# Kernel optimization log

Hardware: AMD Instinct MI355X
Metric: run time of the kernel (lower is better)

## Reference

```python
import jax, jax.numpy as jnp
import numpy as np

B, T, E, H = 64, 577, 768, 64
GRID_H, GRID_W = 24, 24
NUM_PREFIX = 1
N = GRID_H * GRID_W  # 576 patches
EPS = 1e-5


def setup_inputs() -> dict:
    key = jax.random.key(0)
    ks = jax.random.split(key, 12)
    s = lambda k, shape, fan: jax.random.normal(k, shape, jnp.float32) / np.sqrt(fan)
    return {
        "x": jax.random.normal(ks[0], (B, T, E), jnp.float32),
        "w_q": s(ks[1], (E, H), E),
        "w_k": s(ks[2], (E, H), E),
        "w_v": s(ks[3], (E, H), E),
        "q_gamma": jnp.ones((H,), jnp.float32),
        "q_beta": jnp.zeros((H,), jnp.float32),
        "k_gamma": jnp.ones((H,), jnp.float32),
        "k_beta": jnp.zeros((H,), jnp.float32),
        "w_sigma": s(ks[4], (H, 2), H),
        "b_sigma": jnp.zeros((2,), jnp.float32),
        "w_alpha": s(ks[5], (H, 1), H),
        "b_alpha": jnp.zeros((1,), jnp.float32),
    }


def _layernorm(x, gamma, beta):
    mu = jnp.mean(x, axis=-1, keepdims=True)
    var = jnp.mean(jnp.square(x - mu), axis=-1, keepdims=True)
    return (x - mu) * jax.lax.rsqrt(var + EPS) * gamma + beta


def _grid_sq_dists():
    # coords[i] = (row, col) of patch i; squared coordinate differences [N, N]
    coords = jnp.stack(
        jnp.meshgrid(jnp.arange(GRID_H), jnp.arange(GRID_W), indexing="ij"), axis=-1
    ).reshape(N, 2).astype(jnp.float32)
    diff = coords[:, None, :] - coords[None, :, :]  # [N, N, 2]
    dy2 = jnp.square(diff[..., 0])  # row diff squared
    dx2 = jnp.square(diff[..., 1])  # col diff squared
    return dx2, dy2


def reference(x, w_q, w_k, w_v, q_gamma, q_beta, k_gamma, k_beta,
              w_sigma, b_sigma, w_alpha, b_alpha):
    q = _layernorm(x @ w_q, q_gamma, q_beta)  # [B, T, H]
    k = _layernorm(x @ w_k, k_gamma, k_beta)  # [B, T, H]
    v = x @ w_v                               # [B, T, H]

    sim = jnp.einsum("bqh,bkh->bqk", q, k)    # [B, T, T]

    q_nc = q[:, NUM_PREFIX:, :]               # [B, N, H]
    alpha = jax.nn.softplus(q_nc @ w_alpha + b_alpha)[..., 0]  # [B, N]
    sigma = jax.nn.sigmoid(q_nc @ w_sigma + b_sigma)           # [B, N, 2]
    sx = sigma[..., 0]  # [B, N]
    sy = sigma[..., 1]

    dx2, dy2 = _grid_sq_dists()  # [N, N] each
    # Gaussian decay bias: query-patch p controls sigma; [B, N, N]
    G = jnp.exp(
        -dx2[None] / (2.0 * jnp.square(sx)[:, :, None])
        - dy2[None] / (2.0 * jnp.square(sy)[:, :, None])
    )
    S = alpha[:, :, None] * G

    sim = sim.at[:, NUM_PREFIX:, NUM_PREFIX:].add(S)

    scale = jnp.sqrt(jnp.float32(H))
    attn = jax.nn.softmax(sim / scale, axis=-1)
    return attn @ v  # [B, T, H]
```

## Files before the change

### kernel.cpp

```cpp
#include <hip/hip_runtime.h>
#include <math.h>

#define B_ 64
#define T_ 577
#define E_ 768
#define H_ 64
#define N_ 576
#define GW_ 24

typedef float f32x4 __attribute__((ext_vector_type(4)));
typedef __bf16 bf16x8 __attribute__((ext_vector_type(8)));
typedef __bf16 bf16x4 __attribute__((ext_vector_type(4)));

__device__ inline void split_bf16(float f, __bf16& h, __bf16& l) {
  h = (__bf16)f;
  l = (__bf16)(f - (float)h);
}

__device__ inline float bperm_f(int byte_addr, float x) {
  return __int_as_float(__builtin_amdgcn_ds_bpermute(byte_addr, __float_as_int(x)));
}

__global__ __launch_bounds__(256) void prep_w_kernel(
    const float* __restrict__ wq, const float* __restrict__ wk, const float* __restrict__ wv,
    __bf16* __restrict__ wsw_hi, __bf16* __restrict__ wsw_lo)
{
  int t = blockIdx.x * 256 + threadIdx.x;
  if (t >= 24*192) return;
  int kc = t / 192, n = t - (t/192)*192;
  const float* src = (n < 64) ? wq : ((n < 128) ? wk : wv);
  int nn = n & 63;
  __bf16 hbuf[32], lbuf[32];
  #pragma unroll
  for (int kk = 0; kk < 32; ++kk) {
    float f = src[(size_t)(kc*32 + kk)*64 + nn];
    split_bf16(f, hbuf[kk], lbuf[kk]);
  }
  size_t base = (size_t)t * 32;
  #pragma unroll
  for (int i = 0; i < 4; ++i) {
    *(bf16x8*)(wsw_hi + base + i*8) = *(bf16x8*)&hbuf[i*8];
    *(bf16x8*)(wsw_lo + base + i*8) = *(bf16x8*)&lbuf[i*8];
  }
}

__global__ __launch_bounds__(256) void qkv_ln_kernel(
    const float* __restrict__ x,
    const __bf16* __restrict__ wsw_hi, const __bf16* __restrict__ wsw_lo,
    const float* __restrict__ qg, const float* __restrict__ qb,
    const float* __restrict__ kg, const float* __restrict__ kb,
    const float* __restrict__ wsig, const float* __restrict__ bsig,
    const float* __restrict__ walp, const float* __restrict__ balp,
    float* __restrict__ qo, float* __restrict__ ko, float* __restrict__ vo,
    float* __restrict__ alo, float* __restrict__ sxo, float* __restrict__ syo)
{
  __shared__ __align__(16) float smem[64*193 + 256];
  __bf16* A_hi = (__bf16*)smem;
  __bf16* A_lo = A_hi + 64*40;
  __bf16* B_hi = A_lo + 64*40;
  __bf16* B_lo = B_hi + 192*40;
  float (*Cs)[193] = (float (*)[193])smem;
  float* mu_q = smem + 64*193;
  float* rs_q = mu_q + 64;
  float* mu_k = rs_q + 64;
  float* rs_k = mu_k + 64;

  const int tid  = threadIdx.x;
  const int lane = tid & 63;
  const int w    = tid >> 6;
  const int rowbase = blockIdx.x << 6;

  f32x4 acc[4][3];
  #pragma unroll
  for (int mt = 0; mt < 4; ++mt)
    #pragma unroll
    for (int nt = 0; nt < 3; ++nt)
      acc[mt][nt] = (f32x4){0.f, 0.f, 0.f, 0.f};

  const int m     = lane & 15;
  const int kfrag = (lane >> 4) * 8;

  float4 xr0, xr1;
  bf16x8 whr[3], wlr[3];
  const int s0 = tid, s1 = tid + 256;
  const int arow0 = s0 >> 3, ak0 = (s0 & 7) * 4;
  const int arow1 = s1 >> 3, ak1 = (s1 & 7) * 4;

  auto load_chunk = [&](int kc) {
    xr0 = *(const float4*)(x + (size_t)(rowbase + arow0)*E_ + kc*32 + ak0);
    xr1 = *(const float4*)(x + (size_t)(rowbase + arow1)*E_ + kc*32 + ak1);
    #pragma unroll
    for (int i = 0; i < 3; ++i) {
      int e = tid + 256*i;
      whr[i] = *(const bf16x8*)(wsw_hi + (size_t)kc*6144 + e*8);
      wlr[i] = *(const bf16x8*)(wsw_lo + (size_t)kc*6144 + e*8);
    }
  };
  auto store_chunk = [&]() {
    __bf16 h0,l0,h1,l1,h2,l2,h3,l3;
    split_bf16(xr0.x,h0,l0); split_bf16(xr0.y,h1,l1);
    split_bf16(xr0.z,h2,l2); split_bf16(xr0.w,h3,l3);
    *(bf16x4*)&A_hi[arow0*40 + ak0] = (bf16x4){h0,h1,h2,h3};
    *(bf16x4*)&A_lo[arow0*40 + ak0] = (bf16x4){l0,l1,l2,l3};
    split_bf16(xr1.x,h0,l0); split_bf16(xr1.y,h1,l1);
    split_bf16(xr1.z,h2,l2); split_bf16(xr1.w,h3,l3);
    *(bf16x4*)&A_hi[arow1*40 + ak1] = (bf16x4){h0,h1,h2,h3};
    *(bf16x4*)&A_lo[arow1*40 + ak1] = (bf16x4){l0,l1,l2,l3};
    #pragma unroll
    for (int i = 0; i < 3; ++i) {
      int e = tid + 256*i;
      int n = e >> 2, g = e & 3;
      *(bf16x8*)&B_hi[n*40 + g*8] = whr[i];
      *(bf16x8*)&B_lo[n*40 + g*8] = wlr[i];
    }
  };

  load_chunk(0);
  #pragma unroll 1
  for (int kc = 0; kc < 24; ++kc) {
    __syncthreads();
    store_chunk();
    __syncthreads();
    if (kc < 23) load_chunk(kc + 1);

    bf16x8 bh[3], bl[3];
    #pragma unroll
    for (int nt = 0; nt < 3; ++nt) {
      int n = w*48 + nt*16 + m;
      bh[nt] = *(const bf16x8*)&B_hi[n*40 + kfrag];
      bl[nt] = *(const bf16x8*)&B_lo[n*40 + kfrag];
    }
    #pragma unroll
    for (int mt = 0; mt < 4; ++mt) {
      bf16x8 ah = *(const bf16x8*)&A_hi[(mt*16 + m)*40 + kfrag];
      bf16x8 al = *(const bf16x8*)&A_lo[(mt*16 + m)*40 + kfrag];
      #pragma unroll
      for (int nt = 0; nt < 3; ++nt) {
        acc[mt][nt] = __builtin_amdgcn_mfma_f32_16x16x32_bf16(ah, bh[nt], acc[mt][nt], 0, 0, 0);
        acc[mt][nt] = __builtin_amdgcn_mfma_f32_16x16x32_bf16(al, bh[nt], acc[mt][nt], 0, 0, 0);
        acc[mt][nt] = __builtin_amdgcn_mfma_f32_16x16x32_bf16(ah, bl[nt], acc[mt][nt], 0, 0, 0);
      }
    }
  }
  __syncthreads();

  #pragma unroll
  for (int mt = 0; mt < 4; ++mt)
    #pragma unroll
    for (int nt = 0; nt < 3; ++nt) {
      int row = mt*16 + (lane >> 4)*4;
      int col = w*48 + nt*16 + (lane & 15);
      Cs[row + 0][col] = acc[mt][nt].x;
      Cs[row + 1][col] = acc[mt][nt].y;
      Cs[row + 2][col] = acc[mt][nt].z;
      Cs[row + 3][col] = acc[mt][nt].w;
    }
  __syncthreads();

  if (tid < 64) {
    float s = 0.f;
    for (int h = 0; h < 64; ++h) s += Cs[tid][h];
    float mu = s * (1.f/64.f);
    float vs = 0.f;
    for (int h = 0; h < 64; ++h) { float d = Cs[tid][h] - mu; vs += d*d; }
    mu_q[tid] = mu;
    rs_q[tid] = rsqrtf(vs*(1.f/64.f) + 1e-5f);
  } else if (tid < 128) {
    int r = tid - 64;
    float s = 0.f;
    for (int h = 0; h < 64; ++h) s += Cs[r][64+h];
    float mu = s * (1.f/64.f);
    float vs = 0.f;
    for (int h = 0; h < 64; ++h) { float d = Cs[r][64+h] - mu; vs += d*d; }
    mu_k[r] = mu;
    rs_k[r] = rsqrtf(vs*(1.f/64.f) + 1e-5f);
  }
  __syncthreads();

  if (tid >= 192) {
    int r = tid - 192;
    int mrow = rowbase + r;
    int tindex = mrow % T_;
    if (tindex >= 1) {
      int bb = mrow / T_;
      int g = tindex - 1;
      float mu = mu_q[r], rs = rs_q[r];
      float za = 0.f, z0 = 0.f, z1 = 0.f;
      for (int h = 0; h < 64; ++h) {
        float qv = (Cs[r][h] - mu) * rs * qg[h] + qb[h];
        za += qv * walp[h];
        z0 += qv * wsig[2*h];
        z1 += qv * wsig[2*h+1];
      }
      za += balp[0]; z0 += bsig[0]; z1 += bsig[1];
      float al = fmaxf(za, 0.f) + log1pf(__expf(-fabsf(za)));
      float sx = 1.f/(1.f + __expf(-z0));
      float sy = 1.f/(1.f + __expf(-z1));
      alo[bb*N_ + g] = al;
      sxo[bb*N_ + g] = 0.5f/(sx*sx);
      syo[bb*N_ + g] = 0.5f/(sy*sy);
    }
  }
  for (int idx = tid; idx < 64*48; idx += 256) {
    int r = idx / 48, c4 = (idx - (idx/48)*48) * 4;
    size_t row = (size_t)rowbase + r;
    float4 val = make_float4(Cs[r][c4], Cs[r][c4+1], Cs[r][c4+2], Cs[r][c4+3]);
    if (c4 < 64) {
      float mu = mu_q[r], rs = rs_q[r];
      float4 o;
      o.x = (val.x - mu)*rs*qg[c4+0] + qb[c4+0];
      o.y = (val.y - mu)*rs*qg[c4+1] + qb[c4+1];
      o.z = (val.z - mu)*rs*qg[c4+2] + qb[c4+2];
      o.w = (val.w - mu)*rs*qg[c4+3] + qb[c4+3];
      *(float4*)(qo + row*64 + c4) = o;
    } else if (c4 < 128) {
      int h = c4 - 64;
      float mu = mu_k[r], rs = rs_k[r];
      float4 o;
      o.x = (val.x - mu)*rs*kg[h+0] + kb[h+0];
      o.y = (val.y - mu)*rs*kg[h+1] + kb[h+1];
      o.z = (val.z - mu)*rs*kg[h+2] + kb[h+2];
      o.w = (val.w - mu)*rs*kg[h+3] + kb[h+3];
      *(float4*)(ko + row*64 + h) = o;
    } else {
      *(float4*)(vo + row*64 + (c4-128)) = val;
    }
  }
}

__global__ __launch_bounds__(256, 4) void attn_kernel(
    const float* __restrict__ q, const float* __restrict__ k, const float* __restrict__ v,
    const float* __restrict__ ala, const float* __restrict__ sxa, const float* __restrict__ sya,
    float* __restrict__ out)
{
  __shared__ __align__(16) __bf16 sm[4*4608];
  __bf16* KH = sm;            __bf16* KL = sm + 4608;
  __bf16* VH = sm + 2*4608;   __bf16* VL = sm + 3*4608;

  const int tid  = threadIdx.x;
  const int lane = tid & 63;
  const int w    = tid >> 6;
  const int quad = lane >> 4;
  const int m    = lane & 15;
  const int b    = blockIdx.y;
  const int qt   = blockIdx.x;

  const float* qbase = q + (size_t)b * T_ * H_;
  const float* kbase = k + (size_t)b * T_ * H_;
  const float* vbase = v + (size_t)b * T_ * H_;

  const int  row    = qt*64 + w*16 + m;
  const int  rowc   = row < T_ ? row : T_ - 1;
  const bool qvalid = row < T_;
  const bool qhas   = (row >= 1) && qvalid;
  float al = 0.f, isx = 0.f, isy = 0.f, qr = 0.f, qc = 0.f;
  {
    int g = qhas ? row - 1 : 0;
    if (qhas) {
      al  = ala[b*N_ + g] * 0.125f;
      isx = sxa[b*N_ + g];
      isy = sya[b*N_ + g];
      int gr = g / GW_;
      qr = (float)gr;
      qc = (float)(g - gr*GW_);
    }
  }

  bf16x8 qh[2], ql[2];
  #pragma unroll
  for (int ks = 0; ks < 2; ++ks) {
    float4 f0 = *(const float4*)(qbase + (size_t)rowc*H_ + ks*32 + quad*8);
    float4 f1 = *(const float4*)(qbase + (size_t)rowc*H_ + ks*32 + quad*8 + 4);
    float fv[8] = {f0.x, f0.y, f0.z, f0.w, f1.x, f1.y, f1.z, f1.w};
    #pragma unroll
    for (int j = 0; j < 8; ++j) {
      float s = fv[j] * 0.125f;
      __bf16 h, l;
      split_bf16(s, h, l);
      qh[ks][j] = h;
      ql[ks][j] = l;
    }
  }

  float mo = -INFINITY, lsum = 0.f;
  f32x4 acc[4];
  #pragma unroll
  for (int nt = 0; nt < 4; ++nt) acc[nt] = (f32x4){0.f, 0.f, 0.f, 0.f};

  const int  addrA = ((2*(quad & 1))*16 + m) * 4;
  const int  addrB = addrA + 64;
  const bool hiNT  = quad >= 2;

  float4 kreg[4];
  float  vreg[16];
  const int d0 = tid & 15, k0 = (tid >> 4) * 4;

  auto load_kv = [&](int kt) {
    #pragma unroll
    for (int i = 0; i < 4; ++i) {
      int s = tid + 256*i;
      int key = s >> 4, c4 = (s & 15)*4;
      int kgl = kt*64 + key;
      int kcl = kgl < T_ ? kgl : T_ - 1;
      kreg[i] = *(const float4*)(kbase + (size_t)kcl*H_ + c4);
    }
    #pragma unroll
    for (int di = 0; di < 4; ++di)
      #pragma unroll
      for (int ki = 0; ki < 4; ++ki) {
        int kgl = kt*64 + k0 + ki;
        int kcl = kgl < T_ ? kgl : T_ - 1;
        vreg[di*4+ki] = vbase[(size_t)kcl*H_ + d0 + 16*di];
      }
  };
  auto store_kv = [&]() {
    #pragma unroll
    for (int i = 0; i < 4; ++i) {
      int s = tid + 256*i;
      int key = s >> 4, c4 = (s & 15)*4;
      __bf16 h0,l0,h1,l1,h2,l2,h3,l3;
      split_bf16(kreg[i].x,h0,l0); split_bf16(kreg[i].y,h1,l1);
      split_bf16(kreg[i].z,h2,l2); split_bf16(kreg[i].w,h3,l3);
      *(bf16x4*)&KH[key*72 + c4] = (bf16x4){h0,h1,h2,h3};
      *(bf16x4*)&KL[key*72 + c4] = (bf16x4){l0,l1,l2,l3};
    }
    #pragma unroll
    for (int di = 0; di < 4; ++di) {
      int dim = d0 + 16*di;
      __bf16 h0,l0,h1,l1,h2,l2,h3,l3;
      split_bf16(vreg[di*4+0],h0,l0); split_bf16(vreg[di*4+1],h1,l1);
      split_bf16(vreg[di*4+2],h2,l2); split_bf16(vreg[di*4+3],h3,l3);
      *(bf16x4*)&VH[dim*72 + k0] = (bf16x4){h0,h1,h2,h3};
      *(bf16x4*)&VL[dim*72 + k0] = (bf16x4){l0,l1,l2,l3};
    }
  };

  load_kv(0);
  #pragma unroll 1
  for (int kt = 0; kt < 10; ++kt) {
    __syncthreads();
    store_kv();
    __syncthreads();
    if (kt < 9) load_kv(kt + 1);

    float s_[4][4];
    #pragma unroll
    for (int nt = 0; nt < 4; ++nt) {
      f32x4 sac = (f32x4){0.f, 0.f, 0.f, 0.f};
      #pragma unroll
      for (int ks = 0; ks < 2; ++ks) {
        const int ko_ = ks*32 + quad*8;
        bf16x8 kh = *(const bf16x8*)&KH[(nt*16 + m)*72 + ko_];
        bf16x8 kl = *(const bf16x8*)&KL[(nt*16 + m)*72 + ko_];
        sac = __builtin_amdgcn_mfma_f32_16x16x32_bf16(kh, qh[ks], sac, 0, 0, 0);
        sac = __builtin_amdgcn_mfma_f32_16x16x32_bf16(kl, qh[ks], sac, 0, 0, 0);
        sac = __builtin_amdgcn_mfma_f32_16x16x32_bf16(kh, ql[ks], sac, 0, 0, 0);
      }
      s_[nt][0] = sac.x; s_[nt][1] = sac.y; s_[nt][2] = sac.z; s_[nt][3] = sac.w;
    }

    #pragma unroll
    for (int nt = 0; nt < 4; ++nt) {
      #pragma unroll
      for (int reg = 0; reg < 4; ++reg) {
        int key = kt*64 + nt*16 + quad*4 + reg;
        float sval = s_[nt][reg];
        float kgf = (float)(key - 1);
        float krf = floorf(kgf * (1.0f/24.0f));
        float kcf = kgf - 24.f*krf;
        float dx = qc - kcf, dy = qr - krf;
        float bias = al * __expf(-(dx*dx*isx + dy*dy*isy));
        bool khas = (key >= 1) && (key < T_);
        sval += (khas && qhas) ? bias : 0.f;
        s_[nt][reg] = (key < T_) ? sval : -1e30f;
      }
    }

    float mx = s_[0][0];
    #pragma unroll
    for (int nt = 0; nt < 4; ++nt)
      #pragma unroll
      for (int reg = 0; reg < 4; ++reg)
        mx = fmaxf(mx, s_[nt][reg]);
    mx = fmaxf(mx, __shfl_xor(mx, 16, 64));
    mx = fmaxf(mx, __shfl_xor(mx, 32, 64));
    float mn = fmaxf(mo, mx);
    float sc = __expf(mo - mn);
    float lt = 0.f;
    #pragma unroll
    for (int nt = 0; nt < 4; ++nt)
      #pragma unroll
      for (int reg = 0; reg < 4; ++reg) {
        float p = __expf(s_[nt][reg] - mn);
        s_[nt][reg] = p;
        lt += p;
      }
    lt += __shfl_xor(lt, 16, 64);
    lt += __shfl_xor(lt, 32, 64);
    lsum = lsum*sc + lt;
    mo = mn;
    #pragma unroll
    for (int nt = 0; nt < 4; ++nt) {
      acc[nt].x *= sc; acc[nt].y *= sc; acc[nt].z *= sc; acc[nt].w *= sc;
    }

    bf16x8 fh[2], fl[2];
    #pragma unroll
    for (int ks = 0; ks < 2; ++ks) {
      #pragma unroll
      for (int reg = 0; reg < 4; ++reg) {
        float xa0 = bperm_f(addrA, s_[2*ks+0][reg]);
        float xa1 = bperm_f(addrA, s_[2*ks+1][reg]);
        float xb0 = bperm_f(addrB, s_[2*ks+0][reg]);
        float xb1 = bperm_f(addrB, s_[2*ks+1][reg]);
        float va = hiNT ? xa1 : xa0;
        float vb = hiNT ? xb1 : xb0;
        __bf16 h, l;
        split_bf16(va, h, l); fh[ks][reg]   = h; fl[ks][reg]   = l;
        split_bf16(vb, h, l); fh[ks][4+reg] = h; fl[ks][4+reg] = l;
      }
    }

    #pragma unroll
    for (int nt = 0; nt < 4; ++nt) {
      f32x4 c = acc[nt];
      #pragma unroll
      for (int ks = 0; ks < 2; ++ks) {
        const int ko_ = ks*32 + quad*8;
        bf16x8 vh = *(const bf16x8*)&VH[(nt*16 + m)*72 + ko_];
        bf16x8 vl = *(const bf16x8*)&VL[(nt*16 + m)*72 + ko_];
        c = __builtin_amdgcn_mfma_f32_16x16x32_bf16(vh, fh[ks], c, 0, 0, 0);
        c = __builtin_amdgcn_mfma_f32_16x16x32_bf16(vl, fh[ks], c, 0, 0, 0);
        c = __builtin_amdgcn_mfma_f32_16x16x32_bf16(vh, fl[ks], c, 0, 0, 0);
      }
      acc[nt] = c;
    }
  }

  if (qvalid) {
    float inv = 1.f / lsum;
    #pragma unroll
    for (int nt = 0; nt < 4; ++nt) {
      float4 o;
      o.x = acc[nt].x * inv;
      o.y = acc[nt].y * inv;
      o.z = acc[nt].z * inv;
      o.w = acc[nt].w * inv;
      *(float4*)(out + ((size_t)b*T_ + row)*H_ + nt*16 + quad*4) = o;
    }
  }
}

extern "C" void kernel_launch(void* const* d_in, const int* in_sizes, int n_in,
                              void* d_out, int out_size, void* d_ws, size_t ws_size,
                              hipStream_t stream) {
  const float* x      = (const float*)d_in[0];
  const float* wq     = (const float*)d_in[1];
  const float* wk     = (const float*)d_in[2];
  const float* wv     = (const float*)d_in[3];
  const float* qg     = (const float*)d_in[4];
  const float* qb     = (const float*)d_in[5];
  const float* kg     = (const float*)d_in[6];
  const float* kb     = (const float*)d_in[7];
  const float* wsig   = (const float*)d_in[8];
  const float* bsig   = (const float*)d_in[9];
  const float* walp   = (const float*)d_in[10];
  const float* balp   = (const float*)d_in[11];
  float* out = (float*)d_out;

  float* ws  = (float*)d_ws;
  const size_t nrow = (size_t)B_ * T_;
  float* qo  = ws;
  float* ko  = qo + nrow*H_;
  float* vo  = ko + nrow*H_;
  float* alo = vo + nrow*H_;
  float* sxo = alo + (size_t)B_*N_;
  float* syo = sxo + (size_t)B_*N_;
  __bf16* wsw_hi = (__bf16*)(syo + (size_t)B_*N_);
  __bf16* wsw_lo = wsw_hi + 24*192*32;

  hipLaunchKernelGGL(prep_w_kernel, dim3(18), dim3(256), 0, stream,
                     wq, wk, wv, wsw_hi, wsw_lo);
  hipLaunchKernelGGL(qkv_ln_kernel, dim3(577), dim3(256), 0, stream,
                     x, wsw_hi, wsw_lo, qg, qb, kg, kb, wsig, bsig, walp, balp,
                     qo, ko, vo, alo, sxo, syo);
  hipLaunchKernelGGL(attn_kernel, dim3(10, B_), dim3(256), 0, stream,
                     qo, ko, vo, alo, sxo, syo, out);
}
```

Baseline: 292.5 us.

## Load MFMA fragments directly from global memory and swizzle attention block order

```diff
diff --git a/kernel.cpp b/kernel.cpp
--- a/kernel.cpp
+++ b/kernel.cpp
@@ -26,25 +26,28 @@
     __bf16* __restrict__ wsw_hi, __bf16* __restrict__ wsw_lo)
 {
   int t = blockIdx.x * 256 + threadIdx.x;
-  if (t >= 24*192) return;
-  int kc = t / 192, n = t - (t/192)*192;
-  const float* src = (n < 64) ? wq : ((n < 128) ? wk : wv);
-  int nn = n & 63;
-  __bf16 hbuf[32], lbuf[32];
+  if (t >= 24*4*3*64) return;
+  int lane  = t & 63;
+  int rest  = t >> 6;
+  int nt    = rest % 3;
+  int rest2 = rest / 3;
+  int w     = rest2 & 3;
+  int ksl   = rest2 >> 2;
+  int col = w*48 + nt*16 + (lane & 15);
+  int k0  = ksl*32 + (lane >> 4)*8;
+  const float* src = (col < 64) ? wq : ((col < 128) ? wk : wv);
+  int cc = col & 63;
+  __bf16 hb[8], lb[8];
   #pragma unroll
-  for (int kk = 0; kk < 32; ++kk) {
-    float f = src[(size_t)(kc*32 + kk)*64 + nn];
-    split_bf16(f, hbuf[kk], lbuf[kk]);
-  }
-  size_t base = (size_t)t * 32;
-  #pragma unroll
-  for (int i = 0; i < 4; ++i) {
-    *(bf16x8*)(wsw_hi + base + i*8) = *(bf16x8*)&hbuf[i*8];
-    *(bf16x8*)(wsw_lo + base + i*8) = *(bf16x8*)&lbuf[i*8];
-  }
-}
-
-__global__ __launch_bounds__(256) void qkv_ln_kernel(
+  for (int j = 0; j < 8; ++j) {
+    float f = src[(size_t)(k0 + j)*64 + cc];
+    split_bf16(f, hb[j], lb[j]);
+  }
+  *(bf16x8*)(wsw_hi + (size_t)t*8) = *(bf16x8*)hb;
+  *(bf16x8*)(wsw_lo + (size_t)t*8) = *(bf16x8*)lb;
+}
+
+__global__ __launch_bounds__(256, 3) void qkv_ln_kernel(
     const float* __restrict__ x,
     const __bf16* __restrict__ wsw_hi, const __bf16* __restrict__ wsw_lo,
     const float* __restrict__ qg, const float* __restrict__ qb,
@@ -55,10 +58,6 @@
     float* __restrict__ alo, float* __restrict__ sxo, float* __restrict__ syo)
 {
   __shared__ __align__(16) float smem[64*193 + 256];
-  __bf16* A_hi = (__bf16*)smem;
-  __bf16* A_lo = A_hi + 64*40;
-  __bf16* B_hi = A_lo + 64*40;
-  __bf16* B_lo = B_hi + 192*40;
   float (*Cs)[193] = (float (*)[193])smem;
   float* mu_q = smem + 64*193;
   float* rs_q = mu_q + 64;
@@ -68,6 +67,8 @@
   const int tid  = threadIdx.x;
   const int lane = tid & 63;
   const int w    = tid >> 6;
+  const int quad = lane >> 4;
+  const int m    = lane & 15;
   const int rowbase = blockIdx.x << 6;
 
   f32x4 acc[4][3];
@@ -77,63 +78,33 @@
     for (int nt = 0; nt < 3; ++nt)
       acc[mt][nt] = (f32x4){0.f, 0.f, 0.f, 0.f};
 
-  const int m     = lane & 15;
-  const int kfrag = (lane >> 4) * 8;
-
-  float4 xr0, xr1;
-  bf16x8 whr[3], wlr[3];
-  const int s0 = tid, s1 = tid + 256;
-  const int arow0 = s0 >> 3, ak0 = (s0 & 7) * 4;
-  const int arow1 = s1 >> 3, ak1 = (s1 & 7) * 4;
-
-  auto load_chunk = [&](int kc) {
-    xr0 = *(const float4*)(x + (size_t)(rowbase + arow0)*E_ + kc*32 + ak0);
-    xr1 = *(const float4*)(x + (size_t)(rowbase + arow1)*E_ + kc*32 + ak1);
-    #pragma unroll
-    for (int i = 0; i < 3; ++i) {
-      int e = tid + 256*i;
-      whr[i] = *(const bf16x8*)(wsw_hi + (size_t)kc*6144 + e*8);
-      wlr[i] = *(const bf16x8*)(wsw_lo + (size_t)kc*6144 + e*8);
-    }
-  };
-  auto store_chunk = [&]() {
-    __bf16 h0,l0,h1,l1,h2,l2,h3,l3;
-    split_bf16(xr0.x,h0,l0); split_bf16(xr0.y,h1,l1);
-    split_bf16(xr0.z,h2,l2); split_bf16(xr0.w,h3,l3);
-    *(bf16x4*)&A_hi[arow0*40 + ak0] = (bf16x4){h0,h1,h2,h3};
-    *(bf16x4*)&A_lo[arow0*40 + ak0] = (bf16x4){l0,l1,l2,l3};
-    split_bf16(xr1.x,h0,l0); split_bf16(xr1.y,h1,l1);
-    split_bf16(xr1.z,h2,l2); split_bf16(xr1.w,h3,l3);
-    *(bf16x4*)&A_hi[arow1*40 + ak1] = (bf16x4){h0,h1,h2,h3};
-    *(bf16x4*)&A_lo[arow1*40 + ak1] = (bf16x4){l0,l1,l2,l3};
-    #pragma unroll
-    for (int i = 0; i < 3; ++i) {
-      int e = tid + 256*i;
-      int n = e >> 2, g = e & 3;
-      *(bf16x8*)&B_hi[n*40 + g*8] = whr[i];
-      *(bf16x8*)&B_lo[n*40 + g*8] = wlr[i];
-    }
-  };
-
-  load_chunk(0);
-  #pragma unroll 1
-  for (int kc = 0; kc < 24; ++kc) {
-    __syncthreads();
-    store_chunk();
-    __syncthreads();
-    if (kc < 23) load_chunk(kc + 1);
-
+  const __bf16* bbase_h = wsw_hi + ((size_t)w*3*64 + lane)*8;
+  const __bf16* bbase_l = wsw_lo + ((size_t)w*3*64 + lane)*8;
+  const float*  abase   = x + (size_t)(rowbase + m)*E_ + quad*8;
+
+  #pragma unroll 2
+  for (int ks = 0; ks < 24; ++ks) {
     bf16x8 bh[3], bl[3];
     #pragma unroll
     for (int nt = 0; nt < 3; ++nt) {
-      int n = w*48 + nt*16 + m;
-      bh[nt] = *(const bf16x8*)&B_hi[n*40 + kfrag];
-      bl[nt] = *(const bf16x8*)&B_lo[n*40 + kfrag];
+      size_t off = ((size_t)ks*12 + nt)*64*8;
+      bh[nt] = *(const bf16x8*)(bbase_h + off);
+      bl[nt] = *(const bf16x8*)(bbase_l + off);
     }
     #pragma unroll
     for (int mt = 0; mt < 4; ++mt) {
-      bf16x8 ah = *(const bf16x8*)&A_hi[(mt*16 + m)*40 + kfrag];
-      bf16x8 al = *(const bf16x8*)&A_lo[(mt*16 + m)*40 + kfrag];
+      const float* xp = abase + (size_t)mt*16*E_ + ks*32;
+      float4 f0 = *(const float4*)xp;
+      float4 f1 = *(const float4*)(xp + 4);
+      float fv[8] = {f0.x, f0.y, f0.z, f0.w, f1.x, f1.y, f1.z, f1.w};
+      bf16x8 ah, al;
+      #pragma unroll
+      for (int j = 0; j < 8; ++j) {
+        __bf16 h, l;
+        split_bf16(fv[j], h, l);
+        ah[j] = h;
+        al[j] = l;
+      }
       #pragma unroll
       for (int nt = 0; nt < 3; ++nt) {
         acc[mt][nt] = __builtin_amdgcn_mfma_f32_16x16x32_bf16(ah, bh[nt], acc[mt][nt], 0, 0, 0);
@@ -142,14 +113,13 @@
       }
     }
   }
-  __syncthreads();
 
   #pragma unroll
   for (int mt = 0; mt < 4; ++mt)
     #pragma unroll
     for (int nt = 0; nt < 3; ++nt) {
-      int row = mt*16 + (lane >> 4)*4;
-      int col = w*48 + nt*16 + (lane & 15);
+      int row = mt*16 + quad*4;
+      int col = w*48 + nt*16 + m;
       Cs[row + 0][col] = acc[mt][nt].x;
       Cs[row + 1][col] = acc[mt][nt].y;
       Cs[row + 2][col] = acc[mt][nt].z;
@@ -242,8 +212,11 @@
   const int w    = tid >> 6;
   const int quad = lane >> 4;
   const int m    = lane & 15;
-  const int b    = blockIdx.y;
-  const int qt   = blockIdx.x;
+
+  const int f       = blockIdx.y * 10 + blockIdx.x;
+  const int logical = (f & 7) * 80 + (f >> 3);
+  const int b       = logical / 10;
+  const int qt      = logical - b * 10;
 
   const float* qbase = q + (size_t)b * T_ * H_;
   const float* kbase = k + (size_t)b * T_ * H_;
@@ -479,7 +452,7 @@
   __bf16* wsw_hi = (__bf16*)(syo + (size_t)B_*N_);
   __bf16* wsw_lo = wsw_hi + 24*192*32;
 
-  hipLaunchKernelGGL(prep_w_kernel, dim3(18), dim3(256), 0, stream,
+  hipLaunchKernelGGL(prep_w_kernel, dim3(72), dim3(256), 0, stream,
                      wq, wk, wv, wsw_hi, wsw_lo);
   hipLaunchKernelGGL(qkv_ln_kernel, dim3(577), dim3(256), 0, stream,
                      x, wsw_hi, wsw_lo, qg, qb, kg, kb, wsig, bsig, walp, balp,
```

After: 317.1 us. +8.4%, slower.

## Double-buffer QKV GEMM prefetch, parallelize LayerNorm stats, remap attention blocks across XCDs

Applied to the files above, without the earlier changes.

```diff
diff --git a/kernel.cpp b/kernel.cpp
--- a/kernel.cpp
+++ b/kernel.cpp
@@ -20,6 +20,12 @@
 __device__ inline float bperm_f(int byte_addr, float x) {
   return __int_as_float(__builtin_amdgcn_ds_bpermute(byte_addr, __float_as_int(x)));
 }
+
+#define BAR_LGKM() do {                                      \
+    asm volatile("s_waitcnt lgkmcnt(0)" ::: "memory");       \
+    __builtin_amdgcn_s_barrier();                            \
+    asm volatile("" ::: "memory");                           \
+  } while (0)
 
 __global__ __launch_bounds__(256) void prep_w_kernel(
     const float* __restrict__ wq, const float* __restrict__ wk, const float* __restrict__ wv,
@@ -54,13 +60,13 @@
     float* __restrict__ qo, float* __restrict__ ko, float* __restrict__ vo,
     float* __restrict__ alo, float* __restrict__ sxo, float* __restrict__ syo)
 {
-  __shared__ __align__(16) float smem[64*193 + 256];
+  __shared__ __align__(16) float smem[10240];
   __bf16* A_hi = (__bf16*)smem;
   __bf16* A_lo = A_hi + 64*40;
   __bf16* B_hi = A_lo + 64*40;
   __bf16* B_lo = B_hi + 192*40;
-  float (*Cs)[193] = (float (*)[193])smem;
-  float* mu_q = smem + 64*193;
+  float (*Cs)[132] = (float (*)[132])smem;
+  float* mu_q = smem + 64*132;
   float* rs_q = mu_q + 64;
   float* mu_k = rs_q + 64;
   float* rs_k = mu_k + 64;
@@ -68,6 +74,8 @@
   const int tid  = threadIdx.x;
   const int lane = tid & 63;
   const int w    = tid >> 6;
+  const int quad = lane >> 4;
+  const int m    = lane & 15;
   const int rowbase = blockIdx.x << 6;
 
   f32x4 acc[4][3];
@@ -77,51 +85,55 @@
     for (int nt = 0; nt < 3; ++nt)
       acc[mt][nt] = (f32x4){0.f, 0.f, 0.f, 0.f};
 
-  const int m     = lane & 15;
-  const int kfrag = (lane >> 4) * 8;
-
-  float4 xr0, xr1;
-  bf16x8 whr[3], wlr[3];
-  const int s0 = tid, s1 = tid + 256;
-  const int arow0 = s0 >> 3, ak0 = (s0 & 7) * 4;
-  const int arow1 = s1 >> 3, ak1 = (s1 & 7) * 4;
-
-  auto load_chunk = [&](int kc) {
-    xr0 = *(const float4*)(x + (size_t)(rowbase + arow0)*E_ + kc*32 + ak0);
-    xr1 = *(const float4*)(x + (size_t)(rowbase + arow1)*E_ + kc*32 + ak1);
+  const int kfrag = quad * 8;
+
+  float4 xrA0, xrA1, xrB0, xrB1;
+  bf16x8 whA[3], wlA[3], whB[3], wlB[3];
+  const int arow0 = tid >> 3, ak0 = (tid & 7) * 4;
+  const int arow1 = (tid + 256) >> 3, ak1 = (tid & 7) * 4;
+
+  auto load_set = [&](int kc, float4& x0, float4& x1, bf16x8* wh, bf16x8* wl) {
+    x0 = *(const float4*)(x + (size_t)(rowbase + arow0)*E_ + kc*32 + ak0);
+    x1 = *(const float4*)(x + (size_t)(rowbase + arow1)*E_ + kc*32 + ak1);
     #pragma unroll
     for (int i = 0; i < 3; ++i) {
       int e = tid + 256*i;
-      whr[i] = *(const bf16x8*)(wsw_hi + (size_t)kc*6144 + e*8);
-      wlr[i] = *(const bf16x8*)(wsw_lo + (size_t)kc*6144 + e*8);
+      wh[i] = *(const bf16x8*)(wsw_hi + (size_t)kc*6144 + e*8);
+      wl[i] = *(const bf16x8*)(wsw_lo + (size_t)kc*6144 + e*8);
     }
   };
-  auto store_chunk = [&]() {
+  auto store_set = [&](float4& x0, float4& x1, bf16x8* wh, bf16x8* wl) {
     __bf16 h0,l0,h1,l1,h2,l2,h3,l3;
-    split_bf16(xr0.x,h0,l0); split_bf16(xr0.y,h1,l1);
-    split_bf16(xr0.z,h2,l2); split_bf16(xr0.w,h3,l3);
+    split_bf16(x0.x,h0,l0); split_bf16(x0.y,h1,l1);
+    split_bf16(x0.z,h2,l2); split_bf16(x0.w,h3,l3);
     *(bf16x4*)&A_hi[arow0*40 + ak0] = (bf16x4){h0,h1,h2,h3};
     *(bf16x4*)&A_lo[arow0*40 + ak0] = (bf16x4){l0,l1,l2,l3};
-    split_bf16(xr1.x,h0,l0); split_bf16(xr1.y,h1,l1);
-    split_bf16(xr1.z,h2,l2); split_bf16(xr1.w,h3,l3);
+    split_bf16(x1.x,h0,l0); split_bf16(x1.y,h1,l1);
+    split_bf16(x1.z,h2,l2); split_bf16(x1.w,h3,l3);
     *(bf16x4*)&A_hi[arow1*40 + ak1] = (bf16x4){h0,h1,h2,h3};
     *(bf16x4*)&A_lo[arow1*40 + ak1] = (bf16x4){l0,l1,l2,l3};
     #pragma unroll
     for (int i = 0; i < 3; ++i) {
       int e = tid + 256*i;
       int n = e >> 2, g = e & 3;
-      *(bf16x8*)&B_hi[n*40 + g*8] = whr[i];
-      *(bf16x8*)&B_lo[n*40 + g*8] = wlr[i];
+      *(bf16x8*)&B_hi[n*40 + g*8] = wh[i];
+      *(bf16x8*)&B_lo[n*40 + g*8] = wl[i];
     }
   };
 
-  load_chunk(0);
+  load_set(0, xrA0, xrA1, whA, wlA);
+  load_set(1, xrB0, xrB1, whB, wlB);
+
   #pragma unroll 1
   for (int kc = 0; kc < 24; ++kc) {
-    __syncthreads();
-    store_chunk();
-    __syncthreads();
-    if (kc < 23) load_chunk(kc + 1);
+    BAR_LGKM();
+    if (kc & 1) store_set(xrB0, xrB1, whB, wlB);
+    else        store_set(xrA0, xrA1, whA, wlA);
+    BAR_LGKM();
+    if (kc + 2 < 24) {
+      if (kc & 1) load_set(kc + 2, xrB0, xrB1, whB, wlB);
+      else        load_set(kc + 2, xrA0, xrA1, whA, wlA);
+    }
 
     bf16x8 bh[3], bl[3];
     #pragma unroll
@@ -142,38 +154,54 @@
       }
     }
   }
-  __syncthreads();
+  BAR_LGKM();
 
   #pragma unroll
   for (int mt = 0; mt < 4; ++mt)
     #pragma unroll
     for (int nt = 0; nt < 3; ++nt) {
-      int row = mt*16 + (lane >> 4)*4;
-      int col = w*48 + nt*16 + (lane & 15);
-      Cs[row + 0][col] = acc[mt][nt].x;
-      Cs[row + 1][col] = acc[mt][nt].y;
-      Cs[row + 2][col] = acc[mt][nt].z;
-      Cs[row + 3][col] = acc[mt][nt].w;
+      int col = w*48 + nt*16 + m;
+      int row = mt*16 + quad*4;
+      if (col < 128) {
+        Cs[row + 0][col] = acc[mt][nt].x;
+        Cs[row + 1][col] = acc[mt][nt].y;
+        Cs[row + 2][col] = acc[mt][nt].z;
+        Cs[row + 3][col] = acc[mt][nt].w;
+      } else {
+        int vc = col - 128;
+        size_t gr = (size_t)rowbase + row;
+        vo[(gr + 0)*64 + vc] = acc[mt][nt].x;
+        vo[(gr + 1)*64 + vc] = acc[mt][nt].y;
+        vo[(gr + 2)*64 + vc] = acc[mt][nt].z;
+        vo[(gr + 3)*64 + vc] = acc[mt][nt].w;
+      }
     }
   __syncthreads();
 
-  if (tid < 64) {
-    float s = 0.f;
-    for (int h = 0; h < 64; ++h) s += Cs[tid][h];
-    float mu = s * (1.f/64.f);
-    float vs = 0.f;
-    for (int h = 0; h < 64; ++h) { float d = Cs[tid][h] - mu; vs += d*d; }
-    mu_q[tid] = mu;
-    rs_q[tid] = rsqrtf(vs*(1.f/64.f) + 1e-5f);
-  } else if (tid < 128) {
-    int r = tid - 64;
-    float s = 0.f;
-    for (int h = 0; h < 64; ++h) s += Cs[r][64+h];
-    float mu = s * (1.f/64.f);
-    float vs = 0.f;
-    for (int h = 0; h < 64; ++h) { float d = Cs[r][64+h] - mu; vs += d*d; }
-    mu_k[r] = mu;
-    rs_k[r] = rsqrtf(vs*(1.f/64.f) + 1e-5f);
+  {
+    int r = tid >> 2, p = tid & 3;
+    float sq = 0.f, ssq = 0.f, sk = 0.f, ssk = 0.f;
+    #pragma unroll
+    for (int j = 0; j < 4; ++j) {
+      float4 a = *(const float4*)&Cs[r][p*16 + j*4];
+      sq += a.x + a.y + a.z + a.w;
+      ssq += a.x*a.x + a.y*a.y + a.z*a.z + a.w*a.w;
+      float4 b = *(const float4*)&Cs[r][64 + p*16 + j*4];
+      sk += b.x + b.y + b.z + b.w;
+      ssk += b.x*b.x + b.y*b.y + b.z*b.z + b.w*b.w;
+    }
+    sq += __shfl_xor(sq, 1, 64);  sq += __shfl_xor(sq, 2, 64);
+    ssq += __shfl_xor(ssq, 1, 64); ssq += __shfl_xor(ssq, 2, 64);
+    sk += __shfl_xor(sk, 1, 64);  sk += __shfl_xor(sk, 2, 64);
+    ssk += __shfl_xor(ssk, 1, 64); ssk += __shfl_xor(ssk, 2, 64);
+    if (p == 0) {
+      float muq = sq * (1.f/64.f);
+      float muk = sk * (1.f/64.f);
+      mu_q[r] = muq;
+      rs_q[r] = rsqrtf(ssq*(1.f/64.f) - muq*muq + 1e-5f);
+      mu_k[r] = muk;
+      rs_k[r] = rsqrtf(ssk*(1.f/64.f) - muk*muk + 1e-5f);
+    }
   }
   __syncthreads();
 
@@ -201,8 +229,8 @@
       syo[bb*N_ + g] = 0.5f/(sy*sy);
     }
   }
-  for (int idx = tid; idx < 64*48; idx += 256) {
-    int r = idx / 48, c4 = (idx - (idx/48)*48) * 4;
+  for (int idx = tid; idx < 64*32; idx += 256) {
+    int r = idx >> 5, c4 = (idx & 31) * 4;
     size_t row = (size_t)rowbase + r;
     float4 val = make_float4(Cs[r][c4], Cs[r][c4+1], Cs[r][c4+2], Cs[r][c4+3]);
     if (c4 < 64) {
@@ -213,7 +241,7 @@
       o.z = (val.z - mu)*rs*qg[c4+2] + qb[c4+2];
       o.w = (val.w - mu)*rs*qg[c4+3] + qb[c4+3];
       *(float4*)(qo + row*64 + c4) = o;
-    } else if (c4 < 128) {
+    } else {
       int h = c4 - 64;
       float mu = mu_k[r], rs = rs_k[r];
       float4 o;
@@ -222,8 +250,6 @@
       o.z = (val.z - mu)*rs*kg[h+2] + kb[h+2];
       o.w = (val.w - mu)*rs*kg[h+3] + kb[h+3];
       *(float4*)(ko + row*64 + h) = o;
-    } else {
-      *(float4*)(vo + row*64 + (c4-128)) = val;
     }
   }
 }
@@ -242,8 +268,11 @@
   const int w    = tid >> 6;
   const int quad = lane >> 4;
   const int m    = lane & 15;
-  const int b    = blockIdx.y;
-  const int qt   = blockIdx.x;
+
+  const int f       = blockIdx.y * 10 + blockIdx.x;
+  const int logical = (f & 7) * 80 + (f >> 3);
+  const int b       = logical / 10;
+  const int qt      = logical - b * 10;
 
   const float* qbase = q + (size_t)b * T_ * H_;
   const float* kbase = k + (size_t)b * T_ * H_;
```

Result: slower. 324.9 us (+11.1%).
